# Optimization experiments

Measured on AMD Instinct MI355X. Metric: run time of the kernel, lower is better.

Reference implementation:

```python
import jax, jax.numpy as jnp
import numpy as np

E = 4          # num_experts
B = 32         # batch
CIN = 64
COUT = 64
H = 112
WID = 112
K = 3          # kernel size


def setup_inputs() -> dict:
    key = jax.random.key(0)
    k1, k2, k3, k4 = jax.random.split(key, 4)
    x = jax.random.normal(k1, (B, CIN, H, WID), dtype=jnp.float32)
    layer_mask = jax.random.uniform(k2, (B, E), dtype=jnp.float32)
    # per-expert conv weights/biases (kaiming-ish scale)
    W = jax.random.normal(k3, (E, COUT, CIN, K, K), dtype=jnp.float32) * 0.05
    b = jax.random.normal(k4, (E, COUT), dtype=jnp.float32) * 0.05
    return {"x": x, "layer_mask": layer_mask, "W": W, "b": b}


def _conv(x, w):
    # stride 1, padding 1 on both spatial dims (matches nn.Conv2d(k=3, s=1, p=1))
    return jax.lax.conv_general_dilated(
        x, w, window_strides=(1, 1), padding=[(1, 1), (1, 1)],
        dimension_numbers=("NCHW", "OIHW", "NCHW"))


def reference(x, layer_mask, W, b):
    # Loop over the small fixed expert set, accumulating the gated sum to
    # avoid materializing an [E, B, C, H, W] intermediate.
    out = jnp.zeros((B, COUT, H, WID), dtype=x.dtype)
    for e in range(E):
        expert_out = _conv(x, W[e]) + b[e][None, :, None, None]
        gate = layer_mask[:, e][:, None, None, None]  # [B,1,1,1]
        out = out + expert_out * gate
    return out
```

## Files before the change

kernel.cpp:

```cpp
#include <hip/hip_runtime.h>
#include <stdint.h>

#define CIN   64
#define COUT  64
#define HH    112
#define WW    112
#define NEXP  4
#define HW    (HH * WW)

typedef short bf16x8 __attribute__((ext_vector_type(8)));
typedef float f32x16 __attribute__((ext_vector_type(16)));

__device__ inline uint16_t f2bf(float f) {
    uint32_t u = __builtin_bit_cast(uint32_t, f);
    return (uint16_t)((u + 0x7FFFu + ((u >> 16) & 1u)) >> 16);
}

__device__ __forceinline__ void gll16(const uint16_t* g, uint16_t* l) {
    __builtin_amdgcn_global_load_lds(
        (const __attribute__((address_space(1))) uint32_t*)g,
        (__attribute__((address_space(3))) uint32_t*)l, 16, 0, 0);
}

__global__ __launch_bounds__(256)
void prep(const float* __restrict__ x, const float* __restrict__ W,
          const float* __restrict__ bias, const float* __restrict__ mask,
          uint16_t* __restrict__ Xt, uint16_t* __restrict__ Weff,
          float* __restrict__ Beff, int B) {
    const int nxf = B * 114;
    if ((int)blockIdx.x < nxf) {
        __shared__ float lds[CIN][WW + 1];
        const int hp = blockIdx.x % 114;
        const int n  = blockIdx.x / 114;
        const int h  = hp - 1;
        uint16_t* orow = Xt + ((size_t)(n * 114 + hp)) * 114 * 64;

        if (h < 0 || h >= HH) {
            const uint4 z = {0, 0, 0, 0};
            for (int u = threadIdx.x; u < 114 * 8; u += 256)
                *(uint4*)(orow + u * 8) = z;
            return;
        }
        for (int i = threadIdx.x; i < CIN * WW; i += 256) {
            int ci = i / WW, w = i % WW;
            lds[ci][w] = x[((size_t)(n * CIN + ci)) * HW + h * WW + w];
        }
        __syncthreads();
        for (int u = threadIdx.x; u < 114 * 8; u += 256) {
            int wp = u >> 3, cg = u & 7;
            int w = wp - 1;
            union { uint16_t s[8]; uint4 v; } pk;
            if (w < 0 || w >= WW) {
                pk.v = (uint4){0, 0, 0, 0};
            } else {
#pragma unroll
                for (int j = 0; j < 8; ++j) pk.s[j] = f2bf(lds[cg * 8 + j][w]);
            }
            *(uint4*)(orow + (size_t)u * 8) = pk.v;
        }
    } else {
        int idx = (blockIdx.x - nxf) * 256 + threadIdx.x;
        if (idx >= B * 72 * 512) return;
        int j   = idx & 7;
        int co  = (idx >> 3) & 63;
        int g   = (idx >> 9) % 72;
        int n   = idx / (512 * 72);
        int par   = g & 1;
        int kq    = (g >> 1) & 1;
        int khw   = (g >> 2) % 9;
        int phase = (g >> 2) / 9;
        int ci = phase * 32 + (kq * 2 + par) * 8 + j;
        float acc = 0.f;
#pragma unroll
        for (int e = 0; e < NEXP; ++e)
            acc = fmaf(mask[n * NEXP + e],
                       W[((size_t)(e * COUT + co) * CIN + ci) * 9 + khw], acc);
        Weff[idx] = f2bf(acc);
        if (g == 0 && j == 0) {
            float ba = 0.f;
#pragma unroll
            for (int e = 0; e < NEXP; ++e)
                ba = fmaf(mask[n * NEXP + e], bias[e * COUT + co], ba);
            Beff[n * COUT + co] = ba;
        }
    }
}

__device__ inline void compute_phase(const uint16_t* __restrict__ buf,
                                     const uint16_t* __restrict__ wp,
                                     int rowb, int colb, int par,
                                     f32x16& acc00, f32x16& acc01,
                                     f32x16& acc10, f32x16& acc11) {
#pragma unroll 3
    for (int khw = 0; khw < 9; ++khw) {
        const int dh = khw / 3;
        const int dw = khw - dh * 3;
        const int pb0 = (rowb + dh) * 18 + (colb + dw);
        const int pb1 = pb0 + 36;
        const int f0 = (pb0 >> 1) & 3, f1 = (pb1 >> 1) & 3;
        const uint16_t* lp0 = &buf[pb0 * 32];
        const uint16_t* lp1 = &buf[pb1 * 32];
#pragma unroll
        for (int kq = 0; kq < 2; ++kq) {
            const int cgA = kq * 2 + par;
            bf16x8 b0 = *(const bf16x8*)(lp0 + ((cgA ^ f0) << 3));
            bf16x8 b1 = *(const bf16x8*)(lp1 + ((cgA ^ f1) << 3));
            const uint16_t* wk = wp + (size_t)((khw * 2 + kq) * 2) * 512;
            bf16x8 a0 = *(const bf16x8*)(wk);
            bf16x8 a1 = *(const bf16x8*)(wk + 256);
            acc00 = __builtin_amdgcn_mfma_f32_32x32x16_bf16(a0, b0, acc00, 0, 0, 0);
            acc01 = __builtin_amdgcn_mfma_f32_32x32x16_bf16(a0, b1, acc01, 0, 0, 0);
            acc10 = __builtin_amdgcn_mfma_f32_32x32x16_bf16(a1, b0, acc10, 0, 0, 0);
            acc11 = __builtin_amdgcn_mfma_f32_32x32x16_bf16(a1, b1, acc11, 0, 0, 0);
        }
    }
}

__global__ __launch_bounds__(256, 3)
void conv_gll(const uint16_t* __restrict__ Xt, const uint16_t* __restrict__ Weff,
              const float* __restrict__ Beff, float* __restrict__ out,
              int nwg) {
    __shared__ uint16_t ldsx[1296 * 8];

    int bid = blockIdx.x;
    if ((nwg & 7) == 0)
        bid = (bid & 7) * (nwg >> 3) + (bid >> 3);

    const int tid  = threadIdx.x;
    const int lane = tid & 63;
    const int wid  = tid >> 6;
    const int tileIdx = bid % 49;
    const int n  = bid / 49;
    const int th = tileIdx / 7, tw = tileIdx % 7;
    const int h0 = th * 16, w0 = tw * 16;

    const uint16_t* xt_n = Xt + (size_t)n * (114 * 114 * 64);

    const int rowb = wid * 4 + ((lane & 31) >> 4);
    const int colb = lane & 15;
    const int par  = lane >> 5;

    const uint16_t* wbase = Weff + (size_t)n * 36864
                          + (size_t)par * 512 + (size_t)(lane & 31) * 8;

    f32x16 acc00 = {}, acc01 = {}, acc10 = {}, acc11 = {};

#pragma unroll
    for (int phase = 0; phase < 2; ++phase) {
        if (phase) __syncthreads();
#pragma unroll
        for (int it = 0; it < 5; ++it) {
            int v  = it * 256 + tid;
            int pix = v >> 2, s = v & 3;
            int dh = pix / 18, dw = pix - dh * 18;
            int cg = s ^ ((pix >> 1) & 3);
            const uint16_t* src = xt_n
                + ((size_t)(h0 + dh) * 114 + (w0 + dw)) * 64 + phase * 32 + cg * 8;
            uint16_t* dst = ldsx + (size_t)(it * 256 + wid * 64) * 8;
            gll16(src, dst);
        }
        if (tid < 16) {
            int v = 1280 + tid;
            int pix = v >> 2, s = v & 3;
            int dh = pix / 18, dw = pix - dh * 18;
            int cg = s ^ ((pix >> 1) & 3);
            const uint16_t* src = xt_n
                + ((size_t)(h0 + dh) * 114 + (w0 + dw)) * 64 + phase * 32 + cg * 8;
            *(uint4*)(ldsx + (size_t)v * 8) = *(const uint4*)src;
        }
        __syncthreads();

        compute_phase(ldsx, wbase + (size_t)phase * 36 * 512,
                      rowb, colb, par, acc00, acc01, acc10, acc11);
    }

    const float* bptr = Beff + n * 64;
    const int row0 = h0 + rowb;
    const int col  = w0 + colb;
#pragma unroll
    for (int r = 0; r < 16; ++r) {
        const int co = (r & 3) + 8 * (r >> 2) + 4 * par;
        const float bia0 = bptr[co];
        const float bia1 = bptr[co + 32];
        size_t o00 = ((size_t)(n * COUT + co) * HH + row0) * WW + col;
        __builtin_nontemporal_store(acc00[r] + bia0, &out[o00]);
        __builtin_nontemporal_store(acc01[r] + bia0, &out[o00 + 2 * WW]);
        size_t o10 = o00 + (size_t)32 * HW;
        __builtin_nontemporal_store(acc10[r] + bia1, &out[o10]);
        __builtin_nontemporal_store(acc11[r] + bia1, &out[o10 + 2 * WW]);
    }
}

#define COB   8
#define PIX_PER_BLK 256
#define NTILE (HW / PIX_PER_BLK)

__global__ void fold_weights(const float* __restrict__ W,
                             const float* __restrict__ mask,
                             float* __restrict__ Weff, int B) {
    int idx = blockIdx.x * blockDim.x + threadIdx.x;
    int total = B * CIN * 9 * COUT;
    if (idx >= total) return;
    int co = idx % COUT;
    int t  = idx / COUT;
    int k  = t % 9;
    t /= 9;
    int ci = t % CIN;
    int n  = t / CIN;
    float acc = 0.f;
#pragma unroll
    for (int e = 0; e < NEXP; ++e)
        acc = fmaf(mask[n * NEXP + e],
                   W[(((size_t)(e * COUT + co) * CIN + ci) * 9) + k], acc);
    Weff[idx] = acc;
}

__global__ __launch_bounds__(PIX_PER_BLK, 4)
void conv_gated(const float* __restrict__ x,
                const float* __restrict__ mask,
                const float* __restrict__ bias,
                const float* __restrict__ Weff,
                float* __restrict__ out) {
    const int tile = blockIdx.x % NTILE;
    const int cob  = (blockIdx.x / NTILE) % (COUT / COB);
    const int n    = blockIdx.x / (NTILE * (COUT / COB));
    const int p = tile * PIX_PER_BLK + threadIdx.x;
    const int h = p / WW;
    const int w = p % WW;
    const int co0 = cob * COB;

    float acc[COB];
#pragma unroll
    for (int j = 0; j < COB; ++j) {
        float a = 0.f;
#pragma unroll
        for (int e = 0; e < NEXP; ++e)
            a = fmaf(mask[n * NEXP + e], bias[e * COUT + co0 + j], a);
        acc[j] = a;
    }

    const float* xb = x + (((size_t)n * CIN) * HH + h) * WW + w;
    const float* wb = Weff + ((size_t)n * CIN) * 9 * COUT + co0;
    const bool rok0 = (h > 0), rok2 = (h < HH - 1);
    const bool cok0 = (w > 0), cok2 = (w < WW - 1);

    for (int ci = 0; ci < CIN; ++ci) {
        const float* xc = xb + (size_t)ci * HW;
        const float* wc = wb + (size_t)ci * 9 * COUT;
#pragma unroll
        for (int kh = 0; kh < 3; ++kh) {
            const bool rok = (kh == 0) ? rok0 : ((kh == 2) ? rok2 : true);
#pragma unroll
            for (int kw = 0; kw < 3; ++kw) {
                const bool cok = (kw == 0) ? cok0 : ((kw == 2) ? cok2 : true);
                float xv = (rok && cok) ? xc[(kh - 1) * WW + (kw - 1)] : 0.f;
                const float4* wk = (const float4*)(wc + (kh * 3 + kw) * COUT);
                float4 wa = wk[0], wb4 = wk[1];
                acc[0] = fmaf(xv, wa.x, acc[0]);
                acc[1] = fmaf(xv, wa.y, acc[1]);
                acc[2] = fmaf(xv, wa.z, acc[2]);
                acc[3] = fmaf(xv, wa.w, acc[3]);
                acc[4] = fmaf(xv, wb4.x, acc[4]);
                acc[5] = fmaf(xv, wb4.y, acc[5]);
                acc[6] = fmaf(xv, wb4.z, acc[6]);
                acc[7] = fmaf(xv, wb4.w, acc[7]);
            }
        }
    }
    float* ob = out + (((size_t)(n * COUT + co0)) * HH + h) * WW + w;
#pragma unroll
    for (int j = 0; j < COB; ++j)
        ob[(size_t)j * HW] = acc[j];
}

extern "C" void kernel_launch(void* const* d_in, const int* in_sizes, int n_in,
                              void* d_out, int out_size, void* d_ws, size_t ws_size,
                              hipStream_t stream) {
    const float* x    = (const float*)d_in[0];
    const float* mask = (const float*)d_in[1];
    const float* W    = (const float*)d_in[2];
    const float* b    = (const float*)d_in[3];
    float* out = (float*)d_out;

    const int B = in_sizes[0] / (CIN * HW);
    const size_t weffB = (size_t)B * 36864 * 2;
    const size_t beffB = (size_t)B * COUT * 4;
    const size_t xtB   = (size_t)B * 114 * 114 * 64 * 2;
    const size_t need  = weffB + beffB + xtB;

    if (ws_size >= need) {
        uint16_t* Weff = (uint16_t*)d_ws;
        float*    Beff = (float*)((char*)d_ws + weffB);
        uint16_t* Xt   = (uint16_t*)((char*)d_ws + weffB + beffB);
        int foldBlocks = (B * 72 * 512 + 255) / 256;
        prep<<<B * 114 + foldBlocks, 256, 0, stream>>>(x, W, b, mask,
                                                       Xt, Weff, Beff, B);
        const int nwg = B * 49;
        conv_gll<<<nwg, 256, 0, stream>>>(Xt, Weff, Beff, out, nwg);
    } else {
        float* Weff = (float*)d_ws;
        const size_t weff_elems = (size_t)B * CIN * 9 * COUT;
        int foldBlocks = (int)((weff_elems + 255) / 256);
        fold_weights<<<foldBlocks, 256, 0, stream>>>(W, mask, Weff, B);
        conv_gated<<<B * (COUT / COB) * NTILE, PIX_PER_BLK, 0, stream>>>(
            x, mask, b, Weff, out);
    }
}
```

Before: 82.63 us.

## Double-buffer input tile in 16-channel quarters to overlap loads with MFMA

```diff
diff --git a/kernel.cpp b/kernel.cpp
--- a/kernel.cpp
+++ b/kernel.cpp
@@ -86,33 +86,56 @@
     }
 }
 
-__device__ inline void compute_phase(const uint16_t* __restrict__ buf,
-                                     const uint16_t* __restrict__ wp,
-                                     int rowb, int colb, int par,
-                                     f32x16& acc00, f32x16& acc01,
-                                     f32x16& acc10, f32x16& acc11) {
+__device__ __forceinline__ void stage_q(const uint16_t* __restrict__ xt_n,
+                                        uint16_t* __restrict__ buf,
+                                        int h0, int w0, int q,
+                                        int tid, int wid) {
+#pragma unroll
+    for (int it = 0; it < 2; ++it) {
+        int v = it * 256 + tid;
+        int pix = v >> 1, s = v & 1;
+        int dh = pix / 18, dw = pix - dh * 18;
+        int o = s ^ ((pix >> 2) & 1);
+        const uint16_t* src = xt_n + ((size_t)(h0 + dh) * 114 + (w0 + dw)) * 64
+                            + q * 16 + o * 8;
+        uint16_t* dst = buf + (size_t)(it * 256 + wid * 64) * 8;
+        gll16(src, dst);
+    }
+    if (wid < 3) {
+        int v = 512 + tid;
+        int pix = v >> 1, s = v & 1;
+        int p = pix > 323 ? 323 : pix;
+        int dh = p / 18, dw = p - dh * 18;
+        int o = s ^ ((p >> 2) & 1);
+        const uint16_t* src = xt_n + ((size_t)(h0 + dh) * 114 + (w0 + dw)) * 64
+                            + q * 16 + o * 8;
+        uint16_t* dst = buf + (size_t)(512 + wid * 64) * 8;
+        gll16(src, dst);
+    }
+}
+
+__device__ __forceinline__ void compute_q(const uint16_t* __restrict__ buf,
+                                          const uint16_t* __restrict__ wq,
+                                          int rowb, int colb, int par,
+                                          f32x16& acc00, f32x16& acc01,
+                                          f32x16& acc10, f32x16& acc11) {
 #pragma unroll 3
     for (int khw = 0; khw < 9; ++khw) {
         const int dh = khw / 3;
         const int dw = khw - dh * 3;
         const int pb0 = (rowb + dh) * 18 + (colb + dw);
         const int pb1 = pb0 + 36;
-        const int f0 = (pb0 >> 1) & 3, f1 = (pb1 >> 1) & 3;
-        const uint16_t* lp0 = &buf[pb0 * 32];
-        const uint16_t* lp1 = &buf[pb1 * 32];
-#pragma unroll
-        for (int kq = 0; kq < 2; ++kq) {
-            const int cgA = kq * 2 + par;
-            bf16x8 b0 = *(const bf16x8*)(lp0 + ((cgA ^ f0) << 3));
-            bf16x8 b1 = *(const bf16x8*)(lp1 + ((cgA ^ f1) << 3));
-            const uint16_t* wk = wp + (size_t)((khw * 2 + kq) * 2) * 512;
-            bf16x8 a0 = *(const bf16x8*)(wk);
-            bf16x8 a1 = *(const bf16x8*)(wk + 256);
-            acc00 = __builtin_amdgcn_mfma_f32_32x32x16_bf16(a0, b0, acc00, 0, 0, 0);
-            acc01 = __builtin_amdgcn_mfma_f32_32x32x16_bf16(a0, b1, acc01, 0, 0, 0);
-            acc10 = __builtin_amdgcn_mfma_f32_32x32x16_bf16(a1, b0, acc10, 0, 0, 0);
-            acc11 = __builtin_amdgcn_mfma_f32_32x32x16_bf16(a1, b1, acc11, 0, 0, 0);
-        }
+        bf16x8 b0 = *(const bf16x8*)(buf + pb0 * 16
+                      + ((par ^ ((pb0 >> 2) & 1)) << 3));
+        bf16x8 b1 = *(const bf16x8*)(buf + pb1 * 16
+                      + ((par ^ ((pb1 >> 2) & 1)) << 3));
+        const uint16_t* wk = wq + (size_t)(khw * 4) * 512;
+        bf16x8 a0 = *(const bf16x8*)(wk);
+        bf16x8 a1 = *(const bf16x8*)(wk + 256);
+        acc00 = __builtin_amdgcn_mfma_f32_32x32x16_bf16(a0, b0, acc00, 0, 0, 0);
+        acc01 = __builtin_amdgcn_mfma_f32_32x32x16_bf16(a0, b1, acc01, 0, 0, 0);
+        acc10 = __builtin_amdgcn_mfma_f32_32x32x16_bf16(a1, b0, acc10, 0, 0, 0);
+        acc11 = __builtin_amdgcn_mfma_f32_32x32x16_bf16(a1, b1, acc11, 0, 0, 0);
     }
 }
 
@@ -120,7 +143,7 @@
 void conv_gll(const uint16_t* __restrict__ Xt, const uint16_t* __restrict__ Weff,
               const float* __restrict__ Beff, float* __restrict__ out,
               int nwg) {
-    __shared__ uint16_t ldsx[1296 * 8];
+    __shared__ uint16_t ldsx[2][704 * 8];
 
     int bid = blockIdx.x;
     if ((nwg & 7) == 0)
@@ -142,37 +165,25 @@
 
     const uint16_t* wbase = Weff + (size_t)n * 36864
                           + (size_t)par * 512 + (size_t)(lane & 31) * 8;
+    const uint16_t* wq0 = wbase;
+    const uint16_t* wq1 = wbase + 2 * 512;
+    const uint16_t* wq2 = wbase + 36 * 512;
+    const uint16_t* wq3 = wbase + 38 * 512;
 
     f32x16 acc00 = {}, acc01 = {}, acc10 = {}, acc11 = {};
 
-#pragma unroll
-    for (int phase = 0; phase < 2; ++phase) {
-        if (phase) __syncthreads();
-#pragma unroll
-        for (int it = 0; it < 5; ++it) {
-            int v  = it * 256 + tid;
-            int pix = v >> 2, s = v & 3;
-            int dh = pix / 18, dw = pix - dh * 18;
-            int cg = s ^ ((pix >> 1) & 3);
-            const uint16_t* src = xt_n
-                + ((size_t)(h0 + dh) * 114 + (w0 + dw)) * 64 + phase * 32 + cg * 8;
-            uint16_t* dst = ldsx + (size_t)(it * 256 + wid * 64) * 8;
-            gll16(src, dst);
-        }
-        if (tid < 16) {
-            int v = 1280 + tid;
-            int pix = v >> 2, s = v & 3;
-            int dh = pix / 18, dw = pix - dh * 18;
-            int cg = s ^ ((pix >> 1) & 3);
-            const uint16_t* src = xt_n
-                + ((size_t)(h0 + dh) * 114 + (w0 + dw)) * 64 + phase * 32 + cg * 8;
-            *(uint4*)(ldsx + (size_t)v * 8) = *(const uint4*)src;
-        }
-        __syncthreads();
-
-        compute_phase(ldsx, wbase + (size_t)phase * 36 * 512,
-                      rowb, colb, par, acc00, acc01, acc10, acc11);
-    }
+    stage_q(xt_n, ldsx[0], h0, w0, 0, tid, wid);
+    __syncthreads();
+    stage_q(xt_n, ldsx[1], h0, w0, 1, tid, wid);
+    compute_q(ldsx[0], wq0, rowb, colb, par, acc00, acc01, acc10, acc11);
+    __syncthreads();
+    stage_q(xt_n, ldsx[0], h0, w0, 2, tid, wid);
+    compute_q(ldsx[1], wq1, rowb, colb, par, acc00, acc01, acc10, acc11);
+    __syncthreads();
+    stage_q(xt_n, ldsx[1], h0, w0, 3, tid, wid);
+    compute_q(ldsx[0], wq2, rowb, colb, par, acc00, acc01, acc10, acc11);
+    __syncthreads();
+    compute_q(ldsx[1], wq3, rowb, colb, par, acc00, acc01, acc10, acc11);
 
     const float* bptr = Beff + n * 64;
     const int row0 = h0 + rowb;
```

Measured after the change: 83.91 us. About the same (+1.6%).

## Halve conv spatial tile to 8x16 and raise occupancy to six blocks

Applied to the files above, without the earlier changes.

```diff
diff --git a/kernel.cpp b/kernel.cpp
--- a/kernel.cpp
+++ b/kernel.cpp
@@ -86,41 +86,11 @@
     }
 }
 
-__device__ inline void compute_phase(const uint16_t* __restrict__ buf,
-                                     const uint16_t* __restrict__ wp,
-                                     int rowb, int colb, int par,
-                                     f32x16& acc00, f32x16& acc01,
-                                     f32x16& acc10, f32x16& acc11) {
-#pragma unroll 3
-    for (int khw = 0; khw < 9; ++khw) {
-        const int dh = khw / 3;
-        const int dw = khw - dh * 3;
-        const int pb0 = (rowb + dh) * 18 + (colb + dw);
-        const int pb1 = pb0 + 36;
-        const int f0 = (pb0 >> 1) & 3, f1 = (pb1 >> 1) & 3;
-        const uint16_t* lp0 = &buf[pb0 * 32];
-        const uint16_t* lp1 = &buf[pb1 * 32];
-#pragma unroll
-        for (int kq = 0; kq < 2; ++kq) {
-            const int cgA = kq * 2 + par;
-            bf16x8 b0 = *(const bf16x8*)(lp0 + ((cgA ^ f0) << 3));
-            bf16x8 b1 = *(const bf16x8*)(lp1 + ((cgA ^ f1) << 3));
-            const uint16_t* wk = wp + (size_t)((khw * 2 + kq) * 2) * 512;
-            bf16x8 a0 = *(const bf16x8*)(wk);
-            bf16x8 a1 = *(const bf16x8*)(wk + 256);
-            acc00 = __builtin_amdgcn_mfma_f32_32x32x16_bf16(a0, b0, acc00, 0, 0, 0);
-            acc01 = __builtin_amdgcn_mfma_f32_32x32x16_bf16(a0, b1, acc01, 0, 0, 0);
-            acc10 = __builtin_amdgcn_mfma_f32_32x32x16_bf16(a1, b0, acc10, 0, 0, 0);
-            acc11 = __builtin_amdgcn_mfma_f32_32x32x16_bf16(a1, b1, acc11, 0, 0, 0);
-        }
-    }
-}
-
-__global__ __launch_bounds__(256, 3)
+__global__ __launch_bounds__(256, 6)
 void conv_gll(const uint16_t* __restrict__ Xt, const uint16_t* __restrict__ Weff,
               const float* __restrict__ Beff, float* __restrict__ out,
               int nwg) {
-    __shared__ uint16_t ldsx[1296 * 8];
+    __shared__ uint16_t ldsx[720 * 8];
 
     int bid = blockIdx.x;
     if ((nwg & 7) == 0)
@@ -129,49 +99,65 @@
     const int tid  = threadIdx.x;
     const int lane = tid & 63;
     const int wid  = tid >> 6;
-    const int tileIdx = bid % 49;
-    const int n  = bid / 49;
+    const int tileIdx = bid % 98;
+    const int n  = bid / 98;
     const int th = tileIdx / 7, tw = tileIdx % 7;
-    const int h0 = th * 16, w0 = tw * 16;
+    const int h0 = th * 8, w0 = tw * 16;
 
     const uint16_t* xt_n = Xt + (size_t)n * (114 * 114 * 64);
 
-    const int rowb = wid * 4 + ((lane & 31) >> 4);
+    const int rowb = wid * 2 + ((lane & 31) >> 4);
     const int colb = lane & 15;
     const int par  = lane >> 5;
 
     const uint16_t* wbase = Weff + (size_t)n * 36864
                           + (size_t)par * 512 + (size_t)(lane & 31) * 8;
 
-    f32x16 acc00 = {}, acc01 = {}, acc10 = {}, acc11 = {};
+    f32x16 acc0 = {}, acc1 = {};
 
 #pragma unroll
     for (int phase = 0; phase < 2; ++phase) {
         if (phase) __syncthreads();
 #pragma unroll
-        for (int it = 0; it < 5; ++it) {
-            int v  = it * 256 + tid;
+        for (int it = 0; it < 2; ++it) {
+            int v = it * 256 + tid;
             int pix = v >> 2, s = v & 3;
             int dh = pix / 18, dw = pix - dh * 18;
-            int cg = s ^ ((pix >> 1) & 3);
+            int o = s ^ ((pix >> 1) & 3);
             const uint16_t* src = xt_n
-                + ((size_t)(h0 + dh) * 114 + (w0 + dw)) * 64 + phase * 32 + cg * 8;
-            uint16_t* dst = ldsx + (size_t)(it * 256 + wid * 64) * 8;
-            gll16(src, dst);
-        }
-        if (tid < 16) {
-            int v = 1280 + tid;
+                + ((size_t)(h0 + dh) * 114 + (w0 + dw)) * 64 + phase * 32 + o * 8;
+            gll16(src, ldsx + (size_t)(it * 256 + wid * 64) * 8);
+        }
+        if (tid < 208) {
+            int v = 512 + tid;
             int pix = v >> 2, s = v & 3;
             int dh = pix / 18, dw = pix - dh * 18;
-            int cg = s ^ ((pix >> 1) & 3);
+            int o = s ^ ((pix >> 1) & 3);
             const uint16_t* src = xt_n
-                + ((size_t)(h0 + dh) * 114 + (w0 + dw)) * 64 + phase * 32 + cg * 8;
-            *(uint4*)(ldsx + (size_t)v * 8) = *(const uint4*)src;
+                + ((size_t)(h0 + dh) * 114 + (w0 + dw)) * 64 + phase * 32 + o * 8;
+            gll16(src, ldsx + (size_t)(512 + wid * 64) * 8);
         }
         __syncthreads();
 
-        compute_phase(ldsx, wbase + (size_t)phase * 36 * 512,
-                      rowb, colb, par, acc00, acc01, acc10, acc11);
+        const uint16_t* wp = wbase + (size_t)phase * 36 * 512;
+#pragma unroll 2
+        for (int khw = 0; khw < 9; ++khw) {
+            const int dh = khw / 3;
+            const int dw = khw - dh * 3;
+            const int pb = (rowb + dh) * 18 + (colb + dw);
+            const int f  = (pb >> 1) & 3;
+            const uint16_t* lp = &ldsx[pb * 32];
+#pragma unroll
+            for (int kq = 0; kq < 2; ++kq) {
+                const int cgA = kq * 2 + par;
+                bf16x8 b0 = *(const bf16x8*)(lp + ((cgA ^ f) << 3));
+                const uint16_t* wk = wp + (size_t)((khw * 2 + kq) * 2) * 512;
+                bf16x8 a0 = *(const bf16x8*)(wk);
+                bf16x8 a1 = *(const bf16x8*)(wk + 256);
+                acc0 = __builtin_amdgcn_mfma_f32_32x32x16_bf16(a0, b0, acc0, 0, 0, 0);
+                acc1 = __builtin_amdgcn_mfma_f32_32x32x16_bf16(a1, b0, acc1, 0, 0, 0);
+            }
+        }
     }
 
     const float* bptr = Beff + n * 64;
@@ -180,14 +166,10 @@
 #pragma unroll
     for (int r = 0; r < 16; ++r) {
         const int co = (r & 3) + 8 * (r >> 2) + 4 * par;
-        const float bia0 = bptr[co];
-        const float bia1 = bptr[co + 32];
-        size_t o00 = ((size_t)(n * COUT + co) * HH + row0) * WW + col;
-        __builtin_nontemporal_store(acc00[r] + bia0, &out[o00]);
-        __builtin_nontemporal_store(acc01[r] + bia0, &out[o00 + 2 * WW]);
-        size_t o10 = o00 + (size_t)32 * HW;
-        __builtin_nontemporal_store(acc10[r] + bia1, &out[o10]);
-        __builtin_nontemporal_store(acc11[r] + bia1, &out[o10 + 2 * WW]);
+        size_t o0 = ((size_t)(n * COUT + co) * HH + row0) * WW + col;
+        __builtin_nontemporal_store(acc0[r] + bptr[co], &out[o0]);
+        __builtin_nontemporal_store(acc1[r] + bptr[co + 32],
+                                    &out[o0 + (size_t)32 * HW]);
     }
 }
 
@@ -295,7 +277,7 @@
         int foldBlocks = (B * 72 * 512 + 255) / 256;
         prep<<<B * 114 + foldBlocks, 256, 0, stream>>>(x, W, b, mask,
                                                        Xt, Weff, Beff, B);
-        const int nwg = B * 49;
+        const int nwg = B * 98;
         conv_gll<<<nwg, 256, 0, stream>>>(Xt, Weff, Beff, out, nwg);
     } else {
         float* Weff = (float*)d_ws;
```

Result: slower. 93.86 us (+13.6%).

## Switch conv to single-wave workgroups on 4x16 pixel tiles

Applied to the files above, without the earlier changes.

```diff
diff --git a/kernel.cpp b/kernel.cpp
--- a/kernel.cpp
+++ b/kernel.cpp
@@ -86,57 +86,25 @@
     }
 }
 
-__device__ inline void compute_phase(const uint16_t* __restrict__ buf,
-                                     const uint16_t* __restrict__ wp,
-                                     int rowb, int colb, int par,
-                                     f32x16& acc00, f32x16& acc01,
-                                     f32x16& acc10, f32x16& acc11) {
-#pragma unroll 3
-    for (int khw = 0; khw < 9; ++khw) {
-        const int dh = khw / 3;
-        const int dw = khw - dh * 3;
-        const int pb0 = (rowb + dh) * 18 + (colb + dw);
-        const int pb1 = pb0 + 36;
-        const int f0 = (pb0 >> 1) & 3, f1 = (pb1 >> 1) & 3;
-        const uint16_t* lp0 = &buf[pb0 * 32];
-        const uint16_t* lp1 = &buf[pb1 * 32];
-#pragma unroll
-        for (int kq = 0; kq < 2; ++kq) {
-            const int cgA = kq * 2 + par;
-            bf16x8 b0 = *(const bf16x8*)(lp0 + ((cgA ^ f0) << 3));
-            bf16x8 b1 = *(const bf16x8*)(lp1 + ((cgA ^ f1) << 3));
-            const uint16_t* wk = wp + (size_t)((khw * 2 + kq) * 2) * 512;
-            bf16x8 a0 = *(const bf16x8*)(wk);
-            bf16x8 a1 = *(const bf16x8*)(wk + 256);
-            acc00 = __builtin_amdgcn_mfma_f32_32x32x16_bf16(a0, b0, acc00, 0, 0, 0);
-            acc01 = __builtin_amdgcn_mfma_f32_32x32x16_bf16(a0, b1, acc01, 0, 0, 0);
-            acc10 = __builtin_amdgcn_mfma_f32_32x32x16_bf16(a1, b0, acc10, 0, 0, 0);
-            acc11 = __builtin_amdgcn_mfma_f32_32x32x16_bf16(a1, b1, acc11, 0, 0, 0);
-        }
-    }
-}
-
-__global__ __launch_bounds__(256, 3)
-void conv_gll(const uint16_t* __restrict__ Xt, const uint16_t* __restrict__ Weff,
-              const float* __restrict__ Beff, float* __restrict__ out,
-              int nwg) {
-    __shared__ uint16_t ldsx[1296 * 8];
+__global__ __launch_bounds__(64, 3)
+void conv_1w(const uint16_t* __restrict__ Xt, const uint16_t* __restrict__ Weff,
+             const float* __restrict__ Beff, float* __restrict__ out,
+             int nwg) {
+    __shared__ uint16_t ldsx[432 * 8];
 
     int bid = blockIdx.x;
     if ((nwg & 7) == 0)
         bid = (bid & 7) * (nwg >> 3) + (bid >> 3);
 
-    const int tid  = threadIdx.x;
-    const int lane = tid & 63;
-    const int wid  = tid >> 6;
-    const int tileIdx = bid % 49;
-    const int n  = bid / 49;
+    const int lane = threadIdx.x;
+    const int tileIdx = bid % 196;
+    const int n  = bid / 196;
     const int th = tileIdx / 7, tw = tileIdx % 7;
-    const int h0 = th * 16, w0 = tw * 16;
+    const int h0 = th * 4, w0 = tw * 16;
 
     const uint16_t* xt_n = Xt + (size_t)n * (114 * 114 * 64);
 
-    const int rowb = wid * 4 + ((lane & 31) >> 4);
+    const int rowb = (lane & 31) >> 4;
     const int colb = lane & 15;
     const int par  = lane >> 5;
 
@@ -149,29 +117,44 @@
     for (int phase = 0; phase < 2; ++phase) {
         if (phase) __syncthreads();
 #pragma unroll
-        for (int it = 0; it < 5; ++it) {
-            int v  = it * 256 + tid;
-            int pix = v >> 2, s = v & 3;
-            int dh = pix / 18, dw = pix - dh * 18;
-            int cg = s ^ ((pix >> 1) & 3);
-            const uint16_t* src = xt_n
-                + ((size_t)(h0 + dh) * 114 + (w0 + dw)) * 64 + phase * 32 + cg * 8;
-            uint16_t* dst = ldsx + (size_t)(it * 256 + wid * 64) * 8;
-            gll16(src, dst);
-        }
-        if (tid < 16) {
-            int v = 1280 + tid;
-            int pix = v >> 2, s = v & 3;
-            int dh = pix / 18, dw = pix - dh * 18;
-            int cg = s ^ ((pix >> 1) & 3);
-            const uint16_t* src = xt_n
-                + ((size_t)(h0 + dh) * 114 + (w0 + dw)) * 64 + phase * 32 + cg * 8;
-            *(uint4*)(ldsx + (size_t)v * 8) = *(const uint4*)src;
+        for (int it = 0; it < 7; ++it) {
+            int v = it * 64 + lane;
+            if (it < 6 || lane < 48) {
+                int pix = v >> 2, s = v & 3;
+                int dh = pix / 18, dw = pix - dh * 18;
+                int o = s ^ ((pix >> 1) & 3);
+                const uint16_t* src = xt_n
+                    + ((size_t)(h0 + dh) * 114 + (w0 + dw)) * 64
+                    + phase * 32 + o * 8;
+                gll16(src, ldsx + (size_t)(it * 64) * 8);
+            }
         }
         __syncthreads();
 
-        compute_phase(ldsx, wbase + (size_t)phase * 36 * 512,
-                      rowb, colb, par, acc00, acc01, acc10, acc11);
+        const uint16_t* wp = wbase + (size_t)phase * 36 * 512;
+#pragma unroll 3
+        for (int khw = 0; khw < 9; ++khw) {
+            const int dh = khw / 3;
+            const int dw = khw - dh * 3;
+            const int pb0 = (rowb + dh) * 18 + (colb + dw);
+            const int pb1 = pb0 + 36;
+            const int f0 = (pb0 >> 1) & 3, f1 = (pb1 >> 1) & 3;
+            const uint16_t* lp0 = &ldsx[pb0 * 32];
+            const uint16_t* lp1 = &ldsx[pb1 * 32];
+#pragma unroll
+            for (int kq = 0; kq < 2; ++kq) {
+                const int cgA = kq * 2 + par;
+                bf16x8 b0 = *(const bf16x8*)(lp0 + ((cgA ^ f0) << 3));
+                bf16x8 b1 = *(const bf16x8*)(lp1 + ((cgA ^ f1) << 3));
+                const uint16_t* wk = wp + (size_t)((khw * 2 + kq) * 2) * 512;
+                bf16x8 a0 = *(const bf16x8*)(wk);
+                bf16x8 a1 = *(const bf16x8*)(wk + 256);
+                acc00 = __builtin_amdgcn_mfma_f32_32x32x16_bf16(a0, b0, acc00, 0, 0, 0);
+                acc01 = __builtin_amdgcn_mfma_f32_32x32x16_bf16(a0, b1, acc01, 0, 0, 0);
+                acc10 = __builtin_amdgcn_mfma_f32_32x32x16_bf16(a1, b0, acc10, 0, 0, 0);
+                acc11 = __builtin_amdgcn_mfma_f32_32x32x16_bf16(a1, b1, acc11, 0, 0, 0);
+            }
+        }
     }
 
     const float* bptr = Beff + n * 64;
@@ -295,8 +278,8 @@
         int foldBlocks = (B * 72 * 512 + 255) / 256;
         prep<<<B * 114 + foldBlocks, 256, 0, stream>>>(x, W, b, mask,
                                                        Xt, Weff, Beff, B);
-        const int nwg = B * 49;
-        conv_gll<<<nwg, 256, 0, stream>>>(Xt, Weff, Beff, out, nwg);
+        const int nwg = B * 196;
+        conv_1w<<<nwg, 64, 0, stream>>>(Xt, Weff, Beff, out, nwg);
     } else {
         float* Weff = (float*)d_ws;
         const size_t weff_elems = (size_t)B * CIN * 9 * COUT;
```

Result: no change. 82.49 us (-0.2%).
